# Kernel optimization log

Measured on AMD Instinct MI355X. Metric: run time of the kernel, lower is better.

## Reference

```python
import jax, jax.numpy as jnp
import numpy as np

N_BUILDINGS = 4096
NUM_CLUSTERS = 128
EMBED_DIM = 128
TEMPORAL_DIM = 24


def setup_inputs() -> dict:
    key = jax.random.key(0)
    ks = jax.random.split(key, 12)
    E, N, C, T = EMBED_DIM, N_BUILDINGS, NUM_CLUSTERS, TEMPORAL_DIM

    def lin(k, fi, fo):
        k1, k2 = jax.random.split(k)
        w = jax.random.normal(k1, (fo, fi), jnp.float32) / np.sqrt(fi).astype(np.float32)
        b = jax.random.normal(k2, (fo,), jnp.float32) * 0.01
        return w, b

    fp_w1, fp_b1 = lin(ks[0], 2 * E + 2, 128)
    fp_w2, fp_b2 = lin(ks[1], 128, 64)
    fp_w3, fp_b3 = lin(ks[2], 64, 1)
    en_w1, en_b1 = lin(ks[3], 1, 16)
    en_w2, en_b2 = lin(ks[4], 16, 1)
    ps_w1, ps_b1 = lin(ks[5], E, 32)
    ps_w2, ps_b2 = lin(ks[6], 32, 1)

    embeddings = jax.random.normal(ks[7], (1, N, E), jnp.float32)
    generation = jax.random.uniform(ks[8], (1, N, T), jnp.float32) * 50.0
    consumption = jax.random.uniform(ks[9], (1, N, T), jnp.float32) * 50.0
    positions = jax.random.uniform(ks[10], (1, N, 2), jnp.float32) * 1000.0
    cluster_assignments = (jnp.arange(N) % C)[None, :].astype(jnp.int32)

    return dict(embeddings=embeddings, generation=generation, consumption=consumption,
                positions=positions,
                fp_w1=fp_w1, fp_b1=fp_b1, fp_w2=fp_w2, fp_b2=fp_b2, fp_w3=fp_w3, fp_b3=fp_b3,
                en_w1=en_w1, en_b1=en_b1, en_w2=en_w2, en_b2=en_b2,
                ps_w1=ps_w1, ps_b1=ps_b1, ps_w2=ps_w2, ps_b2=ps_b2,
                cluster_assignments=cluster_assignments, num_clusters=C, current_hour=12)


def _greedy_cluster(net0, prio, effm, pf):
    """Greedy allocation within one cluster. net0,prio: [K]; effm,pf: [K,K].
    Surplus rows and deficit cols are both visited in descending priority order;
    non-surplus rows have avail=0 and non-deficit cols have needed<=0, matching the
    original code's subset selection + break/continue semantics."""
    K = net0.shape[0]
    order = jnp.argsort(-prio)
    inv = jnp.argsort(order)
    net_o = net0[order]
    eff_o = effm[order][:, order]
    pf_o = pf[order][:, order]

    def outer(dnet, i):
        avail0 = jnp.maximum(net_o[i], 0.0)  # surplus net is never mutated

        def inner(carry, j):
            avail, dn = carry
            needed = -dn[j]
            active = (avail > 0.0) & (needed > 0.0)
            f = jnp.where(active, jnp.minimum(jnp.minimum(avail, needed), pf_o[i, j]), 0.0)
            dn = dn.at[j].add(f * eff_o[i, j])  # deficit receives delivered flow
            return (avail - f, dn), (f, active)

        (_, dnet), (frow, arow) = jax.lax.scan(inner, (avail0, dnet), jnp.arange(K))
        return dnet, (frow, arow)

    dnet, (flows_o, act_o) = jax.lax.scan(outer, net_o, jnp.arange(K))
    return flows_o[inv][:, inv], act_o[inv][:, inv], dnet[inv]


def _forward(embeddings, generation, consumption, positions,
             fp_w1, fp_b1, fp_w2, fp_b2, fp_w3, fp_b3,
             en_w1, en_b1, en_w2, en_b2,
             ps_w1, ps_b1, ps_w2, ps_b2,
             cluster_assignments, num_clusters, current_hour):
    B, N, E = embeddings.shape
    C = num_clusters
    K = N // C
    net = generation[0, :, current_hour] - consumption[0, :, current_hour]  # [N]

    g = jnp.argsort(cluster_assignments[0]).reshape(C, K)  # [C,K] building ids per cluster
    emb_c = embeddings[0][g]   # [C,K,E]
    pos_c = positions[0][g]    # [C,K,2]
    net_c = net[g]             # [C,K]

    # priority scorer (eval mode)
    h = jax.nn.relu(emb_c @ ps_w1.T + ps_b1)
    prio_c = jax.nn.sigmoid(h @ ps_w2.T + ps_b2)[..., 0]  # [C,K]

    # pairwise distances within cluster
    dist = jnp.linalg.norm(pos_c[:, :, None, :] - pos_c[:, None, :, :], axis=-1)  # [C,K,K]

    # efficiency net: eff = 0.85 + 0.13*sigmoid(MLP(dist/1000))
    eh = jax.nn.relu((dist / 1000.0)[..., None] * en_w1[:, 0] + en_b1)  # [C,K,K,16]
    eff = 0.85 + 0.13 * jax.nn.sigmoid(eh @ en_w2.T + en_b2)[..., 0]    # [C,K,K]

    # flow predictor on concat([emb_i, emb_j, dist, hour/24]); split W1 to avoid
    # materializing the [C,K,K,2E+2] feature tensor. Dropout is eval-mode identity.
    W1a, W1b = fp_w1[:, :E], fp_w1[:, E:2 * E]
    w1d, w1h = fp_w1[:, 2 * E], fp_w1[:, 2 * E + 1]
    hi = emb_c @ W1a.T  # [C,K,128]
    hj = emb_c @ W1b.T  # [C,K,128]
    hour_f = current_hour / 24.0
    h1 = jax.nn.relu(hi[:, :, None, :] + hj[:, None, :, :] + dist[..., None] * w1d + hour_f * w1h + fp_b1)
    h2 = jax.nn.relu(h1 @ fp_w2.T + fp_b2)
    pflow = jax.nn.softplus(h2 @ fp_w3.T + fp_b3)[..., 0]  # [C,K,K]

    flows_c, act_c, dnet_c = jax.vmap(_greedy_cluster)(net_c, prio_c, eff, pflow)

    sharing = jnp.zeros((N, N), embeddings.dtype).at[g[:, :, None], g[:, None, :]].set(flows_c)
    effmat = jnp.ones((N, N), embeddings.dtype).at[g[:, :, None], g[:, None, :]].set(
        jnp.where(act_c, eff, 1.0))
    net_after = jnp.zeros((N,), embeddings.dtype).at[g].set(dnet_c)

    sharing = sharing[None]
    effmat = effmat[None]
    total_shared = sharing.sum()
    energy_sent = sharing.sum(axis=2)
    energy_received = (sharing * effmat).sum(axis=1)
    return sharing, effmat, total_shared, energy_sent, energy_received, net_after[None]


def reference(embeddings, generation, consumption, positions,
              fp_w1, fp_b1, fp_w2, fp_b2, fp_w3, fp_b3,
              en_w1, en_b1, en_w2, en_b2,
              ps_w1, ps_b1, ps_w2, ps_b2,
              cluster_assignments, num_clusters, current_hour):
    return _forward(embeddings, generation, consumption, positions,
                    fp_w1, fp_b1, fp_w2, fp_b2, fp_w3, fp_b3,
                    en_w1, en_b1, en_w2, en_b2,
                    ps_w1, ps_b1, ps_w2, ps_b2,
                    cluster_assignments, num_clusters, current_hour)
```

## Files before the change

kernel.cpp:

```cpp
#include <hip/hip_runtime.h>
#include <math.h>

#define NB 4096
#define NC 128
#define NK 32
#define NE 128

typedef __bf16 bf16x8 __attribute__((ext_vector_type(8)));
typedef float floatx4 __attribute__((ext_vector_type(4)));

__device__ __forceinline__ float sigmoidf_(float x){
  if (x >= 0.f){ float z = expf(-x); return 1.f/(1.f+z); }
  float z = expf(x); return z/(1.f+z);
}
__device__ __forceinline__ float softplusf_(float x){
  return fmaxf(x, 0.f) + log1pf(expf(-fabsf(x)));
}
__device__ __forceinline__ unsigned int pack_bf16(float a, float b){
  unsigned short ua = __builtin_bit_cast(unsigned short, (__bf16)a);
  unsigned short ub = __builtin_bit_cast(unsigned short, (__bf16)b);
  return (unsigned int)ua | ((unsigned int)ub << 16);
}

__global__ void k_prep_group(const float* __restrict__ fp_w1, const float* __restrict__ ps_w1,
                             const float* __restrict__ fp_b1, const float* __restrict__ fp_w2,
                             const int* __restrict__ assign, const int* __restrict__ hourp,
                             float* __restrict__ w1at, float* __restrict__ w1bt,
                             float* __restrict__ ps_w1t, int* __restrict__ g,
                             int* __restrict__ row_of, float* __restrict__ w1d_c,
                             float* __restrict__ bzc, uint4* __restrict__ w2f,
                             float* __restrict__ total){
  int bid = blockIdx.x;
  int t = threadIdx.x;
  if (bid < 80){
    int idx = bid*256 + t;
    if (idx < 128*128){
      int o = idx >> 7, e = idx & 127;
      w1at[e*128 + o] = fp_w1[o*258 + e];
      w1bt[e*128 + o] = fp_w1[o*258 + 128 + e];
    } else {
      int i2 = idx - 128*128;
      if (i2 < 128*32){
        int e = i2 >> 5, q = i2 & 31;
        ps_w1t[e*32 + q] = ps_w1[q*128 + e];
      }
    }
  } else if (bid < 96){
    __shared__ int hist[NC];
    __shared__ int loc[256];
    int start = (bid - 80)*256;
    for (int c = t; c < NC; c += 256) hist[c] = 0;
    __syncthreads();
    for (int j = t; j < start; j += 256) atomicAdd(&hist[assign[j]], 1);
    int i = start + t;
    int c = assign[i];
    loc[t] = c;
    __syncthreads();
    int r = hist[c];
    for (int j = 0; j < 256; ++j) r += (j < t && loc[j] == c) ? 1 : 0;
    if (r >= NK) r = NK - 1;
    g[c*NK + r] = i;
    row_of[i] = c*NK + r;
  } else if (bid == 96){
    if (t < 128){
      float hour_f = (float)hourp[0] / 24.0f;
      w1d_c[t] = fp_w1[t*258 + 256];
      bzc[t]   = fmaf(hour_f, fp_w1[t*258 + 257], fp_b1[t]);
    }
    if (t == 128) total[0] = 0.f;
  } else {
    for (int ff = t; ff < 1024; ff += 256){
      int lane = ff & 63, fi = ff >> 6;
      int nt = fi >> 2, ks = fi & 3;
      int o = nt*16 + (lane & 15);
      int kb = ks*32 + (lane >> 4)*8;
      const float* src = fp_w2 + o*128 + kb;
      uint4 u;
      u.x = pack_bf16(src[0], src[1]);
      u.y = pack_bf16(src[2], src[3]);
      u.z = pack_bf16(src[4], src[5]);
      u.w = pack_bf16(src[6], src[7]);
      w2f[ff] = u;
    }
  }
}

__global__ void k_hijprio(const float* __restrict__ emb, const float* __restrict__ gen,
                          const float* __restrict__ cons, const float* __restrict__ pos,
                          const float* __restrict__ w1at, const float* __restrict__ w1bt,
                          const float* __restrict__ ps_w1t, const float* __restrict__ ps_b1,
                          const float* __restrict__ ps_w2, const float* __restrict__ ps_b2,
                          const int* __restrict__ row_of, const int* __restrict__ hourp,
                          float* __restrict__ hi_c, float* __restrict__ hj_c,
                          float* __restrict__ net_c, float* __restrict__ prio_c,
                          float* __restrict__ pos_c){
  __shared__ float es[8*132];
  __shared__ float wsm[128*32];
  int t = threadIdx.x;
  int i0 = blockIdx.x*8;
  for (int idx = t; idx < 8*128; idx += 256){
    int b = idx >> 7, e = idx & 127;
    es[b*132 + e] = emb[(i0 + b)*128 + e];
  }
  for (int idx = t; idx < 128*32; idx += 256) wsm[idx] = ps_w1t[idx];
  __syncthreads();
  {
    int o = t & 127, half = t >> 7;
    float ai[4], aj[4];
#pragma unroll
    for (int r = 0; r < 4; ++r){ ai[r] = 0.f; aj[r] = 0.f; }
    for (int e = 0; e < 128; e += 4){
      float wa0 = w1at[(e+0)*128 + o], wa1 = w1at[(e+1)*128 + o];
      float wa2 = w1at[(e+2)*128 + o], wa3 = w1at[(e+3)*128 + o];
      float wb0 = w1bt[(e+0)*128 + o], wb1 = w1bt[(e+1)*128 + o];
      float wb2 = w1bt[(e+2)*128 + o], wb3 = w1bt[(e+3)*128 + o];
#pragma unroll
      for (int r = 0; r < 4; ++r){
        float4 ev = *(const float4*)&es[(half*4 + r)*132 + e];
        ai[r] = fmaf(ev.x, wa0, fmaf(ev.y, wa1, fmaf(ev.z, wa2, fmaf(ev.w, wa3, ai[r]))));
        aj[r] = fmaf(ev.x, wb0, fmaf(ev.y, wb1, fmaf(ev.z, wb2, fmaf(ev.w, wb3, aj[r]))));
      }
    }
#pragma unroll
    for (int r = 0; r < 4; ++r){
      int b = i0 + half*4 + r;
      int ck = row_of[b];
      hi_c[ck*128 + o] = ai[r];
      hj_c[ck*128 + o] = aj[r];
    }
  }
  {
    int bl = t >> 5, q = t & 31;
    int i = i0 + bl;
    float acc = ps_b1[q];
    const float* er = &es[bl*132];
    for (int e = 0; e < 128; ++e) acc = fmaf(er[e], wsm[e*32 + q], acc);
    float v = fmaxf(acc, 0.f) * ps_w2[q];
    for (int m = 16; m >= 1; m >>= 1) v += __shfl_xor(v, m, 32);
    if (q == 0){
      int ck = row_of[i];
      prio_c[ck] = sigmoidf_(v + ps_b2[0]);
      int h = hourp[0];
      net_c[ck] = gen[i*24 + h] - cons[i*24 + h];
      pos_c[2*ck]   = pos[2*i];
      pos_c[2*ck+1] = pos[2*i+1];
    }
  }
}

__global__ __launch_bounds__(256) void k_pflow(
    const float* __restrict__ hi_c, const float* __restrict__ hj_c,
    const float* __restrict__ pos_c, const float* __restrict__ w1d_c,
    const float* __restrict__ bzc, const uint4* __restrict__ w2f,
    const float* __restrict__ fp_b2, const float* __restrict__ fp_w3,
    const float* __restrict__ fp_b3, float* __restrict__ pflow){
  int t = threadIdx.x;
  int lane = t & 63, wv = t >> 6;
  int gw = blockIdx.x*4 + wv;
  int c = gw >> 6;
  int rem = gw & 63;
  int i = rem >> 1, j0 = (rem & 1)*16;
  int l16 = lane & 15, quad = lane >> 4;
  int j = j0 + l16;
  float xi = pos_c[(c*NK + i)*2 + 0], yi = pos_c[(c*NK + i)*2 + 1];
  float xj = pos_c[(c*NK + j)*2 + 0], yj = pos_c[(c*NK + j)*2 + 1];
  float dx = xi - xj, dy = yi - yj;
  float d = sqrtf(fmaf(dx, dx, dy*dy));
  const float4* hi4 = (const float4*)(hi_c + (c*NK + i)*128);
  const float4* hj4 = (const float4*)(hj_c + (c*NK + j)*128);
  const float4* wd4 = (const float4*)w1d_c;
  const float4* bz4 = (const float4*)bzc;
  bf16x8 af[4];
#pragma unroll
  for (int ks = 0; ks < 4; ++ks){
    int q8 = ks*8 + quad*2;
    float4 a0 = hi4[q8], a1 = hi4[q8 + 1];
    float4 b0 = hj4[q8], b1 = hj4[q8 + 1];
    float4 w0 = wd4[q8], w1 = wd4[q8 + 1];
    float4 z0 = bz4[q8], z1 = bz4[q8 + 1];
    float v0 = fmaxf(a0.x + b0.x + fmaf(d, w0.x, z0.x), 0.f);
    float v1 = fmaxf(a0.y + b0.y + fmaf(d, w0.y, z0.y), 0.f);
    float v2 = fmaxf(a0.z + b0.z + fmaf(d, w0.z, z0.z), 0.f);
    float v3 = fmaxf(a0.w + b0.w + fmaf(d, w0.w, z0.w), 0.f);
    float v4 = fmaxf(a1.x + b1.x + fmaf(d, w1.x, z1.x), 0.f);
    float v5 = fmaxf(a1.y + b1.y + fmaf(d, w1.y, z1.y), 0.f);
    float v6 = fmaxf(a1.z + b1.z + fmaf(d, w1.z, z1.z), 0.f);
    float v7 = fmaxf(a1.w + b1.w + fmaf(d, w1.w, z1.w), 0.f);
    uint4 u;
    u.x = pack_bf16(v0, v1);
    u.y = pack_bf16(v2, v3);
    u.z = pack_bf16(v4, v5);
    u.w = pack_bf16(v6, v7);
    af[ks] = __builtin_bit_cast(bf16x8, u);
  }
  bf16x8 bfr[4][4];
#pragma unroll
  for (int nt = 0; nt < 4; ++nt)
#pragma unroll
    for (int ks = 0; ks < 4; ++ks)
      bfr[nt][ks] = __builtin_bit_cast(bf16x8, w2f[(nt*4 + ks)*64 + lane]);
  floatx4 acc[4];
#pragma unroll
  for (int nt = 0; nt < 4; ++nt){
    acc[nt] = (floatx4){0.f, 0.f, 0.f, 0.f};
#pragma unroll
    for (int ks = 0; ks < 4; ++ks)
      acc[nt] = __builtin_amdgcn_mfma_f32_16x16x32_bf16(af[ks], bfr[nt][ks], acc[nt], 0, 0, 0);
  }
  float b2v[4], w3v[4];
#pragma unroll
  for (int nt = 0; nt < 4; ++nt){
    b2v[nt] = fp_b2[nt*16 + l16];
    w3v[nt] = fp_w3[nt*16 + l16];
  }
  float b3 = fp_b3[0];
#pragma unroll
  for (int r = 0; r < 4; ++r){
    float s = 0.f;
#pragma unroll
    for (int nt = 0; nt < 4; ++nt)
      s = fmaf(fmaxf(acc[nt][r] + b2v[nt], 0.f), w3v[nt], s);
#pragma unroll
    for (int m = 8; m >= 1; m >>= 1) s += __shfl_xor(s, m);
    if (l16 == 0)
      pflow[c*1024 + i*32 + j0 + quad*4 + r] = softplusf_(s + b3);
  }
}

__global__ __launch_bounds__(64) void k_greedy(
    const float* __restrict__ net_c, const float* __restrict__ prio_c,
    const float* __restrict__ pos_c, const float* __restrict__ en_w1,
    const float* __restrict__ en_b1, const float* __restrict__ en_w2,
    const float* __restrict__ en_b2, const float* __restrict__ pflow,
    const int* __restrict__ g,
    float* __restrict__ fl_c, float* __restrict__ ef_c, float* __restrict__ total,
    float* __restrict__ esent, float* __restrict__ erecv, float* __restrict__ nafter){
  __shared__ float pf_s[1024];
  __shared__ float ef_s[1024];
  __shared__ float fl_s[1024];
  __shared__ float efm_s[1024];
  __shared__ float px[32], py[32];
  __shared__ int order_s[32];
  __shared__ int gl[32];
  int t = threadIdx.x;
  int tl = t & 31;
  int c = blockIdx.x;
  for (int e = t; e < 1024; e += 64) pf_s[e] = pflow[c*1024 + e];
  if (t < 32){
    float2 p2 = ((const float2*)pos_c)[c*NK + t];
    px[t] = p2.x; py[t] = p2.y;
    gl[t] = g[c*NK + t];
  }
  __syncthreads();
  for (int e = t; e < 1024; e += 64){
    int ii = e >> 5, jj = e & 31;
    float dx = px[ii] - px[jj], dy = py[ii] - py[jj];
    float d = sqrtf(fmaf(dx, dx, dy*dy));
    float ds = d * (1.0f/1000.0f);
    float acc = en_b2[0];
#pragma unroll
    for (int q = 0; q < 16; ++q)
      acc = fmaf(fmaxf(fmaf(ds, en_w1[q], en_b1[q]), 0.f), en_w2[q], acc);
    ef_s[e] = 0.85f + 0.13f*sigmoidf_(acc);
  }
  float p = (t < 32) ? prio_c[c*NK + t] : -1e30f;
  int rank = 0;
  for (int k = 0; k < 32; ++k){
    float pk = __shfl(p, k, 32);
    rank += ((pk > p) || (pk == p && k < tl)) ? 1 : 0;
  }
  if (t < 32) order_s[rank] = t;
  __syncthreads();
  int b = order_s[tl];
  float net0 = net_c[c*NK + b];
  float dnet = net0;
  float recv = 0.f;
  float ctotal = 0.f;
  for (int i = 0; i < 32; ++i){
    int a = order_s[i];
    float av0 = fmaxf(__shfl(net0, i, 32), 0.f);
    float pf = pf_s[a*32 + b];
    float ef = ef_s[a*32 + b];
    float needed = -dnet;
    float m = (needed > 0.f) ? fminf(needed, pf) : 0.f;
    float s = m;
#pragma unroll
    for (int dd = 1; dd < 32; dd <<= 1){
      float u = __shfl_up(s, dd, 32);
      if (tl >= dd) s += u;
    }
    float Se = __shfl_up(s, 1, 32);
    if (tl == 0) Se = 0.f;
    float rprev = fmaxf(av0 - Se, 0.f);
    int act = (rprev > 0.f) && (needed > 0.f);
    float f = fminf(m, rprev);
    dnet = fmaf(f, ef, dnet);
    recv = fmaf(f, ef, recv);
    if (t < 32){
      fl_s[a*32 + b]  = f;
      efm_s[a*32 + b] = act ? ef : 1.0f;
    }
    float rs = f;
    for (int mm = 16; mm >= 1; mm >>= 1) rs += __shfl_xor(rs, mm, 32);
    if (t == 0){ esent[gl[a]] = rs; ctotal += rs; }
  }
  if (t < 32){
    nafter[gl[b]] = dnet;
    erecv[gl[b]]  = recv;
  }
  if (t == 0) atomicAdd(total, ctotal);
  __syncthreads();
  for (int e = t; e < 1024; e += 64){
    fl_c[c*1024 + e] = fl_s[e];
    ef_c[c*1024 + e] = efm_s[e];
  }
}

__global__ __launch_bounds__(256) void k_write(
    const float* __restrict__ fl_c, const float* __restrict__ ef_c,
    const int* __restrict__ g, const int* __restrict__ row_of,
    float* __restrict__ sharing, float* __restrict__ effm){
  __shared__ float rowS[4096];
  __shared__ float rowE[4096];
  __shared__ int   cols[32];
  __shared__ float vals[32];
  __shared__ float vale[32];
  int t = threadIdx.x;
  int r = blockIdx.x;
  int ra = row_of[r];
  int c = ra >> 5, a = ra & 31;
  if (t < 32){
    cols[t] = g[c*NK + t];
    vals[t] = fl_c[c*1024 + a*32 + t];
    vale[t] = ef_c[c*1024 + a*32 + t];
  }
  float4 z4 = make_float4(0.f, 0.f, 0.f, 0.f);
  float4 o4 = make_float4(1.f, 1.f, 1.f, 1.f);
  float4* s4 = (float4*)rowS;
  float4* e4 = (float4*)rowE;
#pragma unroll
  for (int q = 0; q < 4; ++q){ s4[t + 256*q] = z4; e4[t + 256*q] = o4; }
  __syncthreads();
  if (t < 32){ rowS[cols[t]] = vals[t]; rowE[cols[t]] = vale[t]; }
  __syncthreads();
  float4* gs = (float4*)(sharing + (long)r*NB);
  float4* ge = (float4*)(effm    + (long)r*NB);
#pragma unroll
  for (int q = 0; q < 4; ++q){ gs[t + 256*q] = s4[t + 256*q]; ge[t + 256*q] = e4[t + 256*q]; }
}

extern "C" void kernel_launch(void* const* d_in, const int* in_sizes, int n_in,
                              void* d_out, int out_size, void* d_ws, size_t ws_size,
                              hipStream_t stream){
  (void)in_sizes; (void)n_in; (void)out_size; (void)ws_size;
  const float* emb   = (const float*)d_in[0];
  const float* gen   = (const float*)d_in[1];
  const float* cons  = (const float*)d_in[2];
  const float* pos   = (const float*)d_in[3];
  const float* fp_w1 = (const float*)d_in[4];
  const float* fp_b1 = (const float*)d_in[5];
  const float* fp_w2 = (const float*)d_in[6];
  const float* fp_b2 = (const float*)d_in[7];
  const float* fp_w3 = (const float*)d_in[8];
  const float* fp_b3 = (const float*)d_in[9];
  const float* en_w1 = (const float*)d_in[10];
  const float* en_b1 = (const float*)d_in[11];
  const float* en_w2 = (const float*)d_in[12];
  const float* en_b2 = (const float*)d_in[13];
  const float* ps_w1 = (const float*)d_in[14];
  const float* ps_b1 = (const float*)d_in[15];
  const float* ps_w2 = (const float*)d_in[16];
  const float* ps_b2 = (const float*)d_in[17];
  const int*   assign = (const int*)d_in[18];
  const int*   hourp  = (const int*)d_in[20];

  char* ws = (char*)d_ws;
  float* w1at   = (float*)(ws + 0);
  float* w1bt   = (float*)(ws + 65536);
  float* ps_w1t = (float*)(ws + 131072);
  int*   g      = (int*)  (ws + 147456);
  int*   row_of = (int*)  (ws + 163840);
  float* net_c  = (float*)(ws + 180224);
  float* prio_c = (float*)(ws + 196608);
  float* pos_c  = (float*)(ws + 212992);
  float* w1d_c  = (float*)(ws + 245760);
  float* bzc    = (float*)(ws + 246272);
  float* hi_c   = (float*)(ws + 262144);
  float* hj_c   = (float*)(ws + 2359296);
  float* pflow  = (float*)(ws + 4456448);
  float* fl_c   = (float*)(ws + 4980736);
  float* ef_c   = (float*)(ws + 5505024);
  uint4* w2f    = (uint4*)(ws + 6029312);

  float* sharing = (float*)d_out;
  float* effm    = sharing + (long)NB*NB;
  float* total   = effm + (long)NB*NB;
  float* esent   = total + 1;
  float* erecv   = esent + NB;
  float* nafter  = erecv + NB;

  hipLaunchKernelGGL(k_prep_group, dim3(98), dim3(256), 0, stream,
                     fp_w1, ps_w1, fp_b1, fp_w2, assign, hourp,
                     w1at, w1bt, ps_w1t, g, row_of, w1d_c, bzc, w2f, total);
  hipLaunchKernelGGL(k_hijprio, dim3(512), dim3(256), 0, stream,
                     emb, gen, cons, pos, w1at, w1bt, ps_w1t, ps_b1, ps_w2, ps_b2,
                     row_of, hourp, hi_c, hj_c, net_c, prio_c, pos_c);
  hipLaunchKernelGGL(k_pflow, dim3(2048), dim3(256), 0, stream,
                     hi_c, hj_c, pos_c, w1d_c, bzc, w2f, fp_b2, fp_w3, fp_b3,
                     pflow);
  hipLaunchKernelGGL(k_greedy, dim3(128), dim3(64), 0, stream,
                     net_c, prio_c, pos_c, en_w1, en_b1, en_w2, en_b2, pflow, g,
                     fl_c, ef_c, total, esent, erecv, nafter);
  hipLaunchKernelGGL(k_write, dim3(4096), dim3(256), 0, stream,
                     fl_c, ef_c, g, row_of, sharing, effm);
}
```

Baseline: 264.9 us.

## Fuse prep into hijprio and pflow into greedy, dropping cluster-ordered intermediates

Merges the weight-prep and grouping kernel into the embedding-projection kernel by extending its grid. The projection now reads fp_w1 and ps_w1 directly instead of going through transposed copies. The pairwise flow MLP (MFMA) now runs inside the per-cluster greedy kernel, with 256 threads per cluster writing pflow into shared memory instead of a global buffer. hi/hj/net/prio are stored in building order and gathered through g, which removes the scatter by row_of and the pos_c copy. This cuts two launches and several global round-trips, but pflow now runs on only 128 blocks instead of 2048, and flows are written to global inside the serial greedy loop.

```diff
diff --git a/kernel.cpp b/kernel.cpp
--- a/kernel.cpp
+++ b/kernel.cpp
@@ -22,33 +22,73 @@
   return (unsigned int)ua | ((unsigned int)ub << 16);
 }
 
-__global__ void k_prep_group(const float* __restrict__ fp_w1, const float* __restrict__ ps_w1,
-                             const float* __restrict__ fp_b1, const float* __restrict__ fp_w2,
-                             const int* __restrict__ assign, const int* __restrict__ hourp,
-                             float* __restrict__ w1at, float* __restrict__ w1bt,
-                             float* __restrict__ ps_w1t, int* __restrict__ g,
-                             int* __restrict__ row_of, float* __restrict__ w1d_c,
-                             float* __restrict__ bzc, uint4* __restrict__ w2f,
-                             float* __restrict__ total){
+__global__ void k_hijprio(const float* __restrict__ emb, const float* __restrict__ gen,
+                          const float* __restrict__ cons, const float* __restrict__ fp_w1,
+                          const float* __restrict__ fp_b1, const float* __restrict__ fp_w2,
+                          const float* __restrict__ ps_w1, const float* __restrict__ ps_b1,
+                          const float* __restrict__ ps_w2, const float* __restrict__ ps_b2,
+                          const int* __restrict__ assign, const int* __restrict__ hourp,
+                          float* __restrict__ hi, float* __restrict__ hj,
+                          float* __restrict__ net, float* __restrict__ prio,
+                          int* __restrict__ g, int* __restrict__ row_of,
+                          float* __restrict__ w1d_c, float* __restrict__ bzc,
+                          uint4* __restrict__ w2f, float* __restrict__ total){
   int bid = blockIdx.x;
   int t = threadIdx.x;
-  if (bid < 80){
-    int idx = bid*256 + t;
-    if (idx < 128*128){
-      int o = idx >> 7, e = idx & 127;
-      w1at[e*128 + o] = fp_w1[o*258 + e];
-      w1bt[e*128 + o] = fp_w1[o*258 + 128 + e];
-    } else {
-      int i2 = idx - 128*128;
-      if (i2 < 128*32){
-        int e = i2 >> 5, q = i2 & 31;
-        ps_w1t[e*32 + q] = ps_w1[q*128 + e];
-      }
-    }
-  } else if (bid < 96){
+  if (bid < 512){
+    __shared__ float es[8*132];
+    __shared__ float wsm[128*33];
+    int i0 = bid*8;
+    for (int idx = t; idx < 8*128; idx += 256){
+      int b = idx >> 7, e = idx & 127;
+      es[b*132 + e] = emb[(i0 + b)*128 + e];
+    }
+    for (int idx = t; idx < 4096; idx += 256){
+      int q = idx >> 7, e = idx & 127;
+      wsm[e*33 + q] = ps_w1[q*128 + e];
+    }
+    __syncthreads();
+    {
+      int o = t & 127, half = t >> 7;
+      const float* w1r = fp_w1 + o*258;
+      float ai[4], aj[4];
+#pragma unroll
+      for (int r = 0; r < 4; ++r){ ai[r] = 0.f; aj[r] = 0.f; }
+      for (int e = 0; e < 128; e += 4){
+        float wa0 = w1r[e+0], wa1 = w1r[e+1], wa2 = w1r[e+2], wa3 = w1r[e+3];
+        float wb0 = w1r[128+e+0], wb1 = w1r[128+e+1], wb2 = w1r[128+e+2], wb3 = w1r[128+e+3];
+#pragma unroll
+        for (int r = 0; r < 4; ++r){
+          float4 ev = *(const float4*)&es[(half*4 + r)*132 + e];
+          ai[r] = fmaf(ev.x, wa0, fmaf(ev.y, wa1, fmaf(ev.z, wa2, fmaf(ev.w, wa3, ai[r]))));
+          aj[r] = fmaf(ev.x, wb0, fmaf(ev.y, wb1, fmaf(ev.z, wb2, fmaf(ev.w, wb3, aj[r]))));
+        }
+      }
+#pragma unroll
+      for (int r = 0; r < 4; ++r){
+        int b = i0 + half*4 + r;
+        hi[b*128 + o] = ai[r];
+        hj[b*128 + o] = aj[r];
+      }
+    }
+    {
+      int bl = t >> 5, q = t & 31;
+      int i = i0 + bl;
+      float acc = ps_b1[q];
+      const float* er = &es[bl*132];
+      for (int e = 0; e < 128; ++e) acc = fmaf(er[e], wsm[e*33 + q], acc);
+      float v = fmaxf(acc, 0.f) * ps_w2[q];
+      for (int m = 16; m >= 1; m >>= 1) v += __shfl_xor(v, m, 32);
+      if (q == 0){
+        prio[i] = sigmoidf_(v + ps_b2[0]);
+        int h = hourp[0];
+        net[i] = gen[i*24 + h] - cons[i*24 + h];
+      }
+    }
+  } else if (bid < 528){
     __shared__ int hist[NC];
     __shared__ int loc[256];
-    int start = (bid - 80)*256;
+    int start = (bid - 512)*256;
     for (int c = t; c < NC; c += 256) hist[c] = 0;
     __syncthreads();
     for (int j = t; j < start; j += 256) atomicAdd(&hist[assign[j]], 1);
@@ -61,7 +101,7 @@
     if (r >= NK) r = NK - 1;
     g[c*NK + r] = i;
     row_of[i] = c*NK + r;
-  } else if (bid == 96){
+  } else if (bid == 528){
     if (t < 128){
       float hour_f = (float)hourp[0] / 24.0f;
       w1d_c[t] = fp_w1[t*258 + 256];
@@ -85,174 +125,102 @@
   }
 }
 
-__global__ void k_hijprio(const float* __restrict__ emb, const float* __restrict__ gen,
-                          const float* __restrict__ cons, const float* __restrict__ pos,
-                          const float* __restrict__ w1at, const float* __restrict__ w1bt,
-                          const float* __restrict__ ps_w1t, const float* __restrict__ ps_b1,
-                          const float* __restrict__ ps_w2, const float* __restrict__ ps_b2,
-                          const int* __restrict__ row_of, const int* __restrict__ hourp,
-                          float* __restrict__ hi_c, float* __restrict__ hj_c,
-                          float* __restrict__ net_c, float* __restrict__ prio_c,
-                          float* __restrict__ pos_c){
-  __shared__ float es[8*132];
-  __shared__ float wsm[128*32];
-  int t = threadIdx.x;
-  int i0 = blockIdx.x*8;
-  for (int idx = t; idx < 8*128; idx += 256){
-    int b = idx >> 7, e = idx & 127;
-    es[b*132 + e] = emb[(i0 + b)*128 + e];
-  }
-  for (int idx = t; idx < 128*32; idx += 256) wsm[idx] = ps_w1t[idx];
-  __syncthreads();
-  {
-    int o = t & 127, half = t >> 7;
-    float ai[4], aj[4];
-#pragma unroll
-    for (int r = 0; r < 4; ++r){ ai[r] = 0.f; aj[r] = 0.f; }
-    for (int e = 0; e < 128; e += 4){
-      float wa0 = w1at[(e+0)*128 + o], wa1 = w1at[(e+1)*128 + o];
-      float wa2 = w1at[(e+2)*128 + o], wa3 = w1at[(e+3)*128 + o];
-      float wb0 = w1bt[(e+0)*128 + o], wb1 = w1bt[(e+1)*128 + o];
-      float wb2 = w1bt[(e+2)*128 + o], wb3 = w1bt[(e+3)*128 + o];
-#pragma unroll
-      for (int r = 0; r < 4; ++r){
-        float4 ev = *(const float4*)&es[(half*4 + r)*132 + e];
-        ai[r] = fmaf(ev.x, wa0, fmaf(ev.y, wa1, fmaf(ev.z, wa2, fmaf(ev.w, wa3, ai[r]))));
-        aj[r] = fmaf(ev.x, wb0, fmaf(ev.y, wb1, fmaf(ev.z, wb2, fmaf(ev.w, wb3, aj[r]))));
-      }
-    }
-#pragma unroll
-    for (int r = 0; r < 4; ++r){
-      int b = i0 + half*4 + r;
-      int ck = row_of[b];
-      hi_c[ck*128 + o] = ai[r];
-      hj_c[ck*128 + o] = aj[r];
-    }
-  }
-  {
-    int bl = t >> 5, q = t & 31;
-    int i = i0 + bl;
-    float acc = ps_b1[q];
-    const float* er = &es[bl*132];
-    for (int e = 0; e < 128; ++e) acc = fmaf(er[e], wsm[e*32 + q], acc);
-    float v = fmaxf(acc, 0.f) * ps_w2[q];
-    for (int m = 16; m >= 1; m >>= 1) v += __shfl_xor(v, m, 32);
-    if (q == 0){
-      int ck = row_of[i];
-      prio_c[ck] = sigmoidf_(v + ps_b2[0]);
-      int h = hourp[0];
-      net_c[ck] = gen[i*24 + h] - cons[i*24 + h];
-      pos_c[2*ck]   = pos[2*i];
-      pos_c[2*ck+1] = pos[2*i+1];
-    }
-  }
-}
-
-__global__ __launch_bounds__(256) void k_pflow(
-    const float* __restrict__ hi_c, const float* __restrict__ hj_c,
-    const float* __restrict__ pos_c, const float* __restrict__ w1d_c,
+__global__ __launch_bounds__(256) void k_pfgreedy(
+    const float* __restrict__ hi, const float* __restrict__ hj,
+    const float* __restrict__ pos, const float* __restrict__ net,
+    const float* __restrict__ prio, const float* __restrict__ w1d_c,
     const float* __restrict__ bzc, const uint4* __restrict__ w2f,
     const float* __restrict__ fp_b2, const float* __restrict__ fp_w3,
-    const float* __restrict__ fp_b3, float* __restrict__ pflow){
-  int t = threadIdx.x;
-  int lane = t & 63, wv = t >> 6;
-  int gw = blockIdx.x*4 + wv;
-  int c = gw >> 6;
-  int rem = gw & 63;
-  int i = rem >> 1, j0 = (rem & 1)*16;
-  int l16 = lane & 15, quad = lane >> 4;
-  int j = j0 + l16;
-  float xi = pos_c[(c*NK + i)*2 + 0], yi = pos_c[(c*NK + i)*2 + 1];
-  float xj = pos_c[(c*NK + j)*2 + 0], yj = pos_c[(c*NK + j)*2 + 1];
-  float dx = xi - xj, dy = yi - yj;
-  float d = sqrtf(fmaf(dx, dx, dy*dy));
-  const float4* hi4 = (const float4*)(hi_c + (c*NK + i)*128);
-  const float4* hj4 = (const float4*)(hj_c + (c*NK + j)*128);
-  const float4* wd4 = (const float4*)w1d_c;
-  const float4* bz4 = (const float4*)bzc;
-  bf16x8 af[4];
-#pragma unroll
-  for (int ks = 0; ks < 4; ++ks){
-    int q8 = ks*8 + quad*2;
-    float4 a0 = hi4[q8], a1 = hi4[q8 + 1];
-    float4 b0 = hj4[q8], b1 = hj4[q8 + 1];
-    float4 w0 = wd4[q8], w1 = wd4[q8 + 1];
-    float4 z0 = bz4[q8], z1 = bz4[q8 + 1];
-    float v0 = fmaxf(a0.x + b0.x + fmaf(d, w0.x, z0.x), 0.f);
-    float v1 = fmaxf(a0.y + b0.y + fmaf(d, w0.y, z0.y), 0.f);
-    float v2 = fmaxf(a0.z + b0.z + fmaf(d, w0.z, z0.z), 0.f);
-    float v3 = fmaxf(a0.w + b0.w + fmaf(d, w0.w, z0.w), 0.f);
-    float v4 = fmaxf(a1.x + b1.x + fmaf(d, w1.x, z1.x), 0.f);
-    float v5 = fmaxf(a1.y + b1.y + fmaf(d, w1.y, z1.y), 0.f);
-    float v6 = fmaxf(a1.z + b1.z + fmaf(d, w1.z, z1.z), 0.f);
-    float v7 = fmaxf(a1.w + b1.w + fmaf(d, w1.w, z1.w), 0.f);
-    uint4 u;
-    u.x = pack_bf16(v0, v1);
-    u.y = pack_bf16(v2, v3);
-    u.z = pack_bf16(v4, v5);
-    u.w = pack_bf16(v6, v7);
-    af[ks] = __builtin_bit_cast(bf16x8, u);
-  }
-  bf16x8 bfr[4][4];
-#pragma unroll
-  for (int nt = 0; nt < 4; ++nt)
-#pragma unroll
-    for (int ks = 0; ks < 4; ++ks)
-      bfr[nt][ks] = __builtin_bit_cast(bf16x8, w2f[(nt*4 + ks)*64 + lane]);
-  floatx4 acc[4];
-#pragma unroll
-  for (int nt = 0; nt < 4; ++nt){
-    acc[nt] = (floatx4){0.f, 0.f, 0.f, 0.f};
-#pragma unroll
-    for (int ks = 0; ks < 4; ++ks)
-      acc[nt] = __builtin_amdgcn_mfma_f32_16x16x32_bf16(af[ks], bfr[nt][ks], acc[nt], 0, 0, 0);
-  }
-  float b2v[4], w3v[4];
-#pragma unroll
-  for (int nt = 0; nt < 4; ++nt){
-    b2v[nt] = fp_b2[nt*16 + l16];
-    w3v[nt] = fp_w3[nt*16 + l16];
-  }
-  float b3 = fp_b3[0];
-#pragma unroll
-  for (int r = 0; r < 4; ++r){
-    float s = 0.f;
-#pragma unroll
-    for (int nt = 0; nt < 4; ++nt)
-      s = fmaf(fmaxf(acc[nt][r] + b2v[nt], 0.f), w3v[nt], s);
-#pragma unroll
-    for (int m = 8; m >= 1; m >>= 1) s += __shfl_xor(s, m);
-    if (l16 == 0)
-      pflow[c*1024 + i*32 + j0 + quad*4 + r] = softplusf_(s + b3);
-  }
-}
-
-__global__ __launch_bounds__(64) void k_greedy(
-    const float* __restrict__ net_c, const float* __restrict__ prio_c,
-    const float* __restrict__ pos_c, const float* __restrict__ en_w1,
+    const float* __restrict__ fp_b3, const float* __restrict__ en_w1,
     const float* __restrict__ en_b1, const float* __restrict__ en_w2,
-    const float* __restrict__ en_b2, const float* __restrict__ pflow,
-    const int* __restrict__ g,
+    const float* __restrict__ en_b2, const int* __restrict__ g,
     float* __restrict__ fl_c, float* __restrict__ ef_c, float* __restrict__ total,
     float* __restrict__ esent, float* __restrict__ erecv, float* __restrict__ nafter){
   __shared__ float pf_s[1024];
   __shared__ float ef_s[1024];
-  __shared__ float fl_s[1024];
-  __shared__ float efm_s[1024];
   __shared__ float px[32], py[32];
+  __shared__ int gl[32];
   __shared__ int order_s[32];
-  __shared__ int gl[32];
   int t = threadIdx.x;
-  int tl = t & 31;
+  int lane = t & 63, wv = t >> 6;
   int c = blockIdx.x;
-  for (int e = t; e < 1024; e += 64) pf_s[e] = pflow[c*1024 + e];
   if (t < 32){
-    float2 p2 = ((const float2*)pos_c)[c*NK + t];
-    px[t] = p2.x; py[t] = p2.y;
-    gl[t] = g[c*NK + t];
+    int b = g[c*NK + t];
+    gl[t] = b;
+    px[t] = pos[2*b];
+    py[t] = pos[2*b + 1];
   }
   __syncthreads();
-  for (int e = t; e < 1024; e += 64){
+  {
+    int l16 = lane & 15, quad = lane >> 4;
+    bf16x8 bfr[4][4];
+#pragma unroll
+    for (int nt = 0; nt < 4; ++nt)
+#pragma unroll
+      for (int ks = 0; ks < 4; ++ks)
+        bfr[nt][ks] = __builtin_bit_cast(bf16x8, w2f[(nt*4 + ks)*64 + lane]);
+    float b2v[4], w3v[4];
+#pragma unroll
+    for (int nt = 0; nt < 4; ++nt){
+      b2v[nt] = fp_b2[nt*16 + l16];
+      w3v[nt] = fp_w3[nt*16 + l16];
+    }
+    float b3 = fp_b3[0];
+    const float4* wd4 = (const float4*)w1d_c;
+    const float4* bz4 = (const float4*)bzc;
+    for (int it = 0; it < 16; ++it){
+      int tile = it*4 + wv;
+      int i = tile >> 1, j0 = (tile & 1)*16;
+      int j = j0 + l16;
+      float dx = px[i] - px[j], dy = py[i] - py[j];
+      float d = sqrtf(fmaf(dx, dx, dy*dy));
+      const float4* hi4 = (const float4*)(hi + gl[i]*128);
+      const float4* hj4 = (const float4*)(hj + gl[j]*128);
+      bf16x8 af[4];
+#pragma unroll
+      for (int ks = 0; ks < 4; ++ks){
+        int q8 = ks*8 + quad*2;
+        float4 a0 = hi4[q8], a1 = hi4[q8 + 1];
+        float4 b0 = hj4[q8], b1 = hj4[q8 + 1];
+        float4 w0 = wd4[q8], w1 = wd4[q8 + 1];
+        float4 z0 = bz4[q8], z1 = bz4[q8 + 1];
+        float v0 = fmaxf(a0.x + b0.x + fmaf(d, w0.x, z0.x), 0.f);
+        float v1 = fmaxf(a0.y + b0.y + fmaf(d, w0.y, z0.y), 0.f);
+        float v2 = fmaxf(a0.z + b0.z + fmaf(d, w0.z, z0.z), 0.f);
+        float v3 = fmaxf(a0.w + b0.w + fmaf(d, w0.w, z0.w), 0.f);
+        float v4 = fmaxf(a1.x + b1.x + fmaf(d, w1.x, z1.x), 0.f);
+        float v5 = fmaxf(a1.y + b1.y + fmaf(d, w1.y, z1.y), 0.f);
+        float v6 = fmaxf(a1.z + b1.z + fmaf(d, w1.z, z1.z), 0.f);
+        float v7 = fmaxf(a1.w + b1.w + fmaf(d, w1.w, z1.w), 0.f);
+        uint4 u;
+        u.x = pack_bf16(v0, v1);
+        u.y = pack_bf16(v2, v3);
+        u.z = pack_bf16(v4, v5);
+        u.w = pack_bf16(v6, v7);
+        af[ks] = __builtin_bit_cast(bf16x8, u);
+      }
+      floatx4 acc[4];
+#pragma unroll
+      for (int nt = 0; nt < 4; ++nt){
+        acc[nt] = (floatx4){0.f, 0.f, 0.f, 0.f};
+#pragma unroll
+        for (int ks = 0; ks < 4; ++ks)
+          acc[nt] = __builtin_amdgcn_mfma_f32_16x16x32_bf16(af[ks], bfr[nt][ks], acc[nt], 0, 0, 0);
+      }
+#pragma unroll
+      for (int r = 0; r < 4; ++r){
+        float s = 0.f;
+#pragma unroll
+        for (int nt = 0; nt < 4; ++nt)
+          s = fmaf(fmaxf(acc[nt][r] + b2v[nt], 0.f), w3v[nt], s);
+#pragma unroll
+        for (int m = 8; m >= 1; m >>= 1) s += __shfl_xor(s, m);
+        if (l16 == 0)
+          pf_s[i*32 + j0 + quad*4 + r] = softplusf_(s + b3);
+      }
+    }
+  }
+  for (int e = t; e < 1024; e += 256){
     int ii = e >> 5, jj = e & 31;
     float dx = px[ii] - px[jj], dy = py[ii] - py[jj];
     float d = sqrtf(fmaf(dx, dx, dy*dy));
@@ -263,56 +231,57 @@
       acc = fmaf(fmaxf(fmaf(ds, en_w1[q], en_b1[q]), 0.f), en_w2[q], acc);
     ef_s[e] = 0.85f + 0.13f*sigmoidf_(acc);
   }
-  float p = (t < 32) ? prio_c[c*NK + t] : -1e30f;
-  int rank = 0;
-  for (int k = 0; k < 32; ++k){
-    float pk = __shfl(p, k, 32);
-    rank += ((pk > p) || (pk == p && k < tl)) ? 1 : 0;
-  }
-  if (t < 32) order_s[rank] = t;
+  if (t < 64){
+    int tl = t & 31;
+    float pr = (t < 32) ? prio[gl[t]] : -1e30f;
+    int rank = 0;
+    for (int k = 0; k < 32; ++k){
+      float pk = __shfl(pr, k, 32);
+      rank += ((pk > pr) || (pk == pr && k < tl)) ? 1 : 0;
+    }
+    if (t < 32) order_s[rank] = t;
+  }
   __syncthreads();
-  int b = order_s[tl];
-  float net0 = net_c[c*NK + b];
-  float dnet = net0;
-  float recv = 0.f;
-  float ctotal = 0.f;
-  for (int i = 0; i < 32; ++i){
-    int a = order_s[i];
-    float av0 = fmaxf(__shfl(net0, i, 32), 0.f);
-    float pf = pf_s[a*32 + b];
-    float ef = ef_s[a*32 + b];
-    float needed = -dnet;
-    float m = (needed > 0.f) ? fminf(needed, pf) : 0.f;
-    float s = m;
-#pragma unroll
-    for (int dd = 1; dd < 32; dd <<= 1){
-      float u = __shfl_up(s, dd, 32);
-      if (tl >= dd) s += u;
-    }
-    float Se = __shfl_up(s, 1, 32);
-    if (tl == 0) Se = 0.f;
-    float rprev = fmaxf(av0 - Se, 0.f);
-    int act = (rprev > 0.f) && (needed > 0.f);
-    float f = fminf(m, rprev);
-    dnet = fmaf(f, ef, dnet);
-    recv = fmaf(f, ef, recv);
+  if (t < 64){
+    int tl = t & 31;
+    int b = order_s[tl];
+    float net0 = net[gl[b]];
+    float dnet = net0;
+    float recv = 0.f;
+    float ctotal = 0.f;
+    for (int i = 0; i < 32; ++i){
+      int a = order_s[i];
+      float av0 = fmaxf(__shfl(net0, i, 32), 0.f);
+      float pf = pf_s[a*32 + b];
+      float ef = ef_s[a*32 + b];
+      float needed = -dnet;
+      float m = (needed > 0.f) ? fminf(needed, pf) : 0.f;
+      float s = m;
+#pragma unroll
+      for (int dd = 1; dd < 32; dd <<= 1){
+        float u = __shfl_up(s, dd, 32);
+        if (tl >= dd) s += u;
+      }
+      float Se = __shfl_up(s, 1, 32);
+      if (tl == 0) Se = 0.f;
+      float rprev = fmaxf(av0 - Se, 0.f);
+      int act = (rprev > 0.f) && (needed > 0.f);
+      float f = fminf(m, rprev);
+      dnet = fmaf(f, ef, dnet);
+      recv = fmaf(f, ef, recv);
+      if (t < 32){
+        fl_c[c*1024 + a*32 + b] = f;
+        ef_c[c*1024 + a*32 + b] = act ? ef : 1.0f;
+      }
+      float rs = f;
+      for (int mm = 16; mm >= 1; mm >>= 1) rs += __shfl_xor(rs, mm, 32);
+      if (t == 0){ esent[gl[a]] = rs; ctotal += rs; }
+    }
     if (t < 32){
-      fl_s[a*32 + b]  = f;
-      efm_s[a*32 + b] = act ? ef : 1.0f;
-    }
-    float rs = f;
-    for (int mm = 16; mm >= 1; mm >>= 1) rs += __shfl_xor(rs, mm, 32);
-    if (t == 0){ esent[gl[a]] = rs; ctotal += rs; }
-  }
-  if (t < 32){
-    nafter[gl[b]] = dnet;
-    erecv[gl[b]]  = recv;
-  }
-  if (t == 0) atomicAdd(total, ctotal);
-  __syncthreads();
-  for (int e = t; e < 1024; e += 64){
-    fl_c[c*1024 + e] = fl_s[e];
-    ef_c[c*1024 + e] = efm_s[e];
+      nafter[gl[b]] = dnet;
+      erecv[gl[b]]  = recv;
+    }
+    if (t == 0) atomicAdd(total, ctotal);
   }
 }
 
@@ -375,22 +344,17 @@
   const int*   hourp  = (const int*)d_in[20];
 
   char* ws = (char*)d_ws;
-  float* w1at   = (float*)(ws + 0);
-  float* w1bt   = (float*)(ws + 65536);
-  float* ps_w1t = (float*)(ws + 131072);
-  int*   g      = (int*)  (ws + 147456);
-  int*   row_of = (int*)  (ws + 163840);
-  float* net_c  = (float*)(ws + 180224);
-  float* prio_c = (float*)(ws + 196608);
-  float* pos_c  = (float*)(ws + 212992);
-  float* w1d_c  = (float*)(ws + 245760);
-  float* bzc    = (float*)(ws + 246272);
-  float* hi_c   = (float*)(ws + 262144);
-  float* hj_c   = (float*)(ws + 2359296);
-  float* pflow  = (float*)(ws + 4456448);
-  float* fl_c   = (float*)(ws + 4980736);
-  float* ef_c   = (float*)(ws + 5505024);
-  uint4* w2f    = (uint4*)(ws + 6029312);
+  int*   g      = (int*)  (ws + 0);
+  int*   row_of = (int*)  (ws + 16384);
+  float* net    = (float*)(ws + 32768);
+  float* prio   = (float*)(ws + 49152);
+  float* w1d_c  = (float*)(ws + 65536);
+  float* bzc    = (float*)(ws + 66048);
+  uint4* w2f    = (uint4*)(ws + 131072);
+  float* hi     = (float*)(ws + 262144);
+  float* hj     = (float*)(ws + 2359296);
+  float* fl_c   = (float*)(ws + 4456448);
+  float* ef_c   = (float*)(ws + 4980736);
 
   float* sharing = (float*)d_out;
   float* effm    = sharing + (long)NB*NB;
@@ -399,17 +363,12 @@
   float* erecv   = esent + NB;
   float* nafter  = erecv + NB;
 
-  hipLaunchKernelGGL(k_prep_group, dim3(98), dim3(256), 0, stream,
-                     fp_w1, ps_w1, fp_b1, fp_w2, assign, hourp,
-                     w1at, w1bt, ps_w1t, g, row_of, w1d_c, bzc, w2f, total);
-  hipLaunchKernelGGL(k_hijprio, dim3(512), dim3(256), 0, stream,
-                     emb, gen, cons, pos, w1at, w1bt, ps_w1t, ps_b1, ps_w2, ps_b2,
-                     row_of, hourp, hi_c, hj_c, net_c, prio_c, pos_c);
-  hipLaunchKernelGGL(k_pflow, dim3(2048), dim3(256), 0, stream,
-                     hi_c, hj_c, pos_c, w1d_c, bzc, w2f, fp_b2, fp_w3, fp_b3,
-                     pflow);
-  hipLaunchKernelGGL(k_greedy, dim3(128), dim3(64), 0, stream,
-                     net_c, prio_c, pos_c, en_w1, en_b1, en_w2, en_b2, pflow, g,
+  hipLaunchKernelGGL(k_hijprio, dim3(530), dim3(256), 0, stream,
+                     emb, gen, cons, fp_w1, fp_b1, fp_w2, ps_w1, ps_b1, ps_w2, ps_b2,
+                     assign, hourp, hi, hj, net, prio, g, row_of, w1d_c, bzc, w2f, total);
+  hipLaunchKernelGGL(k_pfgreedy, dim3(128), dim3(256), 0, stream,
+                     hi, hj, pos, net, prio, w1d_c, bzc, w2f, fp_b2, fp_w3, fp_b3,
+                     en_w1, en_b1, en_w2, en_b2, g,
                      fl_c, ef_c, total, esent, erecv, nafter);
   hipLaunchKernelGGL(k_write, dim3(4096), dim3(256), 0, stream,
                      fl_c, ef_c, g, row_of, sharing, effm);
```

New measurement: 263.5 us. Within noise of the previous version (-0.6%).
